# Kernel optimization log

Measured on AMD Instinct MI355X. Metric: run time of the kernel, lower is better.

## Reference

```python
import jax, jax.numpy as jnp
import numpy as np

GH, GW, H, B, IN = 4, 2, 512, 8192, 1
FC_HID = H // 2
NC = GH * GW
BN_EPS = 1e-5


def setup_inputs() -> dict:
    key = jax.random.key(0)
    ks = jax.random.split(key, 20)
    def n(k, shape, s=1.0):
        return jax.random.normal(k, shape, dtype=jnp.float32) * s
    return {
        "x": n(ks[0], (B, GH, GW)),
        "h_ext": n(ks[1], (B, H), 0.1),
        "c_ext": n(ks[2], (B, H), 0.1),
        "grid_h": n(ks[3], (GH, GW, B, H), 0.1),
        "grid_c": n(ks[4], (GH, GW, B, H), 0.1),
        "Wh": n(ks[5], (NC, H, 3 * H), (3 * H) ** -0.5),
        "bh": n(ks[6], (NC, H), 0.01),
        "Wc": n(ks[7], (NC, H, 3 * H), (3 * H) ** -0.5),
        "bc": n(ks[8], (NC, H), 0.01),
        "W_ih": n(ks[9], (NC, 4 * H, IN), 1.0),
        "W_hh": n(ks[10], (NC, 4 * H, H), H ** -0.5),
        "b_ih": n(ks[11], (NC, 4 * H), 0.01),
        "b_hh": n(ks[12], (NC, 4 * H), 0.01),
        "W1": n(ks[13], (FC_HID, 2 * H), (2 * H) ** -0.5),
        "b1": n(ks[14], (FC_HID,), 0.01),
        "W2": n(ks[15], (1, FC_HID), FC_HID ** -0.5),
        "b2": n(ks[16], (1,), 0.01),
        "gamma": jnp.ones((1,), jnp.float32),
        "beta": jnp.zeros((1,), jnp.float32),
    }


def _lattice_forward(x, h_ext, c_ext, grid_h, grid_c, Wh, bh, Wc, bc,
                     W_ih, W_hh, b_ih, b_hh, W1, b1, W2, b2, gamma, beta):
    b = x.shape[0]
    zeros = jnp.zeros((b, H), x.dtype)
    # python lists over the small fixed 4x2 grid (strict left/up dependency)
    sh = [[grid_h[i, j] for j in range(GW)] for i in range(GH)]
    sc = [[grid_c[i, j] for j in range(GW)] for i in range(GH)]
    for i in range(GH):
        for j in range(GW):
            k = i * GW + j
            h_prev, c_prev = sh[i][j], sc[i][j]
            if i == 0 and j == 0:
                h_left, c_left = h_ext, c_ext
            elif j > 0:
                h_left, c_left = sh[i][j - 1], sc[i][j - 1]
            else:
                h_left, c_left = zeros, zeros
            if i > 0:
                h_up, c_up = sh[i - 1][j], sc[i - 1][j]
            else:
                h_up, c_up = zeros, zeros
            comb_h = jnp.concatenate([h_left, h_up, h_prev], axis=1)  # [B,3H]
            comb_c = jnp.concatenate([c_left, c_up, c_prev], axis=1)
            ph = comb_h @ Wh[k].T + bh[k]  # [B,H]
            pc = comb_c @ Wc[k].T + bc[k]
            xi = x[:, i, j][:, None]  # [B,1]
            gates = xi @ W_ih[k].T + b_ih[k] + ph @ W_hh[k].T + b_hh[k]  # [B,4H]
            ig, fg, gg, og = jnp.split(gates, 4, axis=1)
            c_new = jax.nn.sigmoid(fg) * pc + jax.nn.sigmoid(ig) * jnp.tanh(gg)
            h_new = jax.nn.sigmoid(og) * jnp.tanh(c_new)
            sh[i][j], sc[i][j] = h_new, c_new
    final_h = sh[-1][-1] + h_ext
    final_c = sc[-1][-1] + c_ext
    final = jnp.concatenate([final_h, final_c], axis=1)  # [B,2H]
    hid = jax.nn.relu(final @ W1.T + b1)
    out = hid @ W2.T + b2  # [B,1]
    # BatchNorm1d in training mode: biased batch stats over the batch dim
    mu = jnp.mean(out, axis=0, keepdims=True)
    var = jnp.mean((out - mu) ** 2, axis=0, keepdims=True)
    out = gamma * (out - mu) * jax.lax.rsqrt(var + BN_EPS) + beta
    out = jax.nn.sigmoid(out)
    new_gh = jnp.stack([jnp.stack(row) for row in sh])  # [GH,GW,B,H]
    new_gc = jnp.stack([jnp.stack(row) for row in sc])
    return out, final_h, final_c, new_gh, new_gc


def reference(x, h_ext, c_ext, grid_h, grid_c, Wh, bh, Wc, bc,
              W_ih, W_hh, b_ih, b_hh, W1, b1, W2, b2, gamma, beta):
    return _lattice_forward(x, h_ext, c_ext, grid_h, grid_c, Wh, bh, Wc, bc,
                            W_ih, W_hh, b_ih, b_hh, W1, b1, W2, b2, gamma, beta)
```

## Files before the change

### kernel.cpp

```cpp
#include <hip/hip_runtime.h>
#include <stdint.h>

#define B_SZ 8192
static const size_t BH = (size_t)B_SZ * 512;

typedef short bfrag8 __attribute__((ext_vector_type(8)));
typedef float f32x4 __attribute__((ext_vector_type(4)));

__device__ __forceinline__ unsigned short f2bf(float f) {
  union { float f; uint32_t u; } c; c.f = f;
  uint32_t u = c.u;
  uint32_t r = (u + 0x7FFFu + ((u >> 16) & 1u)) >> 16;
  return (unsigned short)r;
}
__device__ __forceinline__ float bf2f(unsigned short u) {
  union { uint32_t u; float f; } c; c.u = ((uint32_t)u) << 16;
  return c.f;
}
__device__ __forceinline__ uint32_t pk2(float a, float b) {
  uint32_t r;
  asm("v_cvt_pk_bf16_f32 %0, %1, %2" : "=v"(r) : "v"(a), "v"(b));
  return r;
}
__device__ __forceinline__ float sigm(float x) { return 1.0f / (1.0f + __expf(-x)); }
__device__ __forceinline__ float tanh_fast(float x) {
  float cx = fminf(fmaxf(x, -15.0f), 15.0f);
  float e = __expf(2.0f * cx);
  return (e - 1.0f) / (e + 1.0f);
}

__device__ __forceinline__ void gload16(const void* g, void* l) {
  __builtin_amdgcn_global_load_lds(
      (const __attribute__((address_space(1))) void*)g,
      (__attribute__((address_space(3))) void*)l, 16, 0, 0);
}

__device__ __forceinline__ void xcd_swizzle(int& bx, int& by, int& bz) {
  int nx = gridDim.x, ny = gridDim.y, nz = gridDim.z;
  int nwg = nx * ny * nz;
  int id = blockIdx.x + nx * (blockIdx.y + ny * blockIdx.z);
  int q = nwg >> 3, r = nwg & 7;
  int xcd = id & 7, lin = id >> 3;
  int swz = (xcd < r ? xcd * (q + 1) : r * (q + 1) + (xcd - r) * q) + lin;
  bx = swz % nx; swz /= nx;
  by = swz % ny; bz = swz / ny;
}

struct PJob {
  const void* A[3];
  int co[3];
  int nseg, relu;
  const unsigned short* B;
  const float* bias;
  unsigned short* outBf;
  unsigned short* outBf2;
};
struct PArgs {
  PJob j[8];
  int ldA, ldB, outStride;
};

template <int AF32>
__global__ __launch_bounds__(256, 4) void pgemm_k(PArgs pa) {
  __shared__ __align__(16) char As[16384];
  __shared__ __align__(16) char Bs[16384];
  int bx, by, bz;
  xcd_swizzle(bx, by, bz);
  const PJob jb = pa.j[bz];
  const int tid = threadIdx.x;
  const int lane = tid & 63;
  const int wv = tid >> 6;
  const int wr = wv >> 1, wc = wv & 1;
  const int m0 = by * 128;
  const int ldA = pa.ldA;

  int rowA[4], cg[4];
  const char* browPtr[4];
#pragma unroll
  for (int q = 0; q < 4; ++q) {
    int cl = q * 256 + tid;
    int row = cl >> 3, cs = cl & 7;
    cg[q] = cs ^ (row & 7);
    rowA[q] = row;
    browPtr[q] = (const char*)jb.B + (size_t)(bx * 128 + row) * pa.ldB * 2;
  }

  f32x4 acc[4][4];
#pragma unroll
  for (int a = 0; a < 4; ++a)
#pragma unroll
    for (int b = 0; b < 4; ++b) acc[a][b] = f32x4{0.f, 0.f, 0.f, 0.f};

  for (int s = 0; s < jb.nseg; ++s) {
    const int coB = jb.co[s] * 2;
    for (int k0 = 0; k0 < 512; k0 += 64) {
#pragma unroll
      for (int q = 0; q < 4; ++q)
        gload16(browPtr[q] + coB + k0 * 2 + cg[q] * 16,
                Bs + (q * 256 + tid) * 16);
      if (AF32) {
        const float* Ab = (const float*)jb.A[s];
#pragma unroll
        for (int q = 0; q < 4; ++q) {
          const float4* p = (const float4*)(Ab + (size_t)(m0 + rowA[q]) * ldA +
                                            k0 + cg[q] * 8);
          float4 a0 = p[0];
          float4 a1 = p[1];
          uint4 w;
          w.x = pk2(a0.x, a0.y);
          w.y = pk2(a0.z, a0.w);
          w.z = pk2(a1.x, a1.y);
          w.w = pk2(a1.z, a1.w);
          *(uint4*)(As + (q * 256 + tid) * 16) = w;
        }
      } else {
        const char* Ab = (const char*)jb.A[s];
#pragma unroll
        for (int q = 0; q < 4; ++q)
          gload16(Ab + ((size_t)(m0 + rowA[q]) * ldA + k0) * 2 + cg[q] * 16,
                  As + (q * 256 + tid) * 16);
      }
      __syncthreads();
#pragma unroll
      for (int ks = 0; ks < 2; ++ks) {
        bfrag8 af[4], bfr[4];
#pragma unroll
        for (int mf = 0; mf < 4; ++mf) {
          int row = wr * 64 + mf * 16 + (lane & 15);
          af[mf] = *(const bfrag8*)(As + row * 128 +
                                    ((ks * 4 + (lane >> 4)) ^ (row & 7)) * 16);
        }
#pragma unroll
        for (int nf = 0; nf < 4; ++nf) {
          int row = wc * 64 + nf * 16 + (lane & 15);
          bfr[nf] = *(const bfrag8*)(Bs + row * 128 +
                                     ((ks * 4 + (lane >> 4)) ^ (row & 7)) * 16);
        }
#pragma unroll
        for (int mf = 0; mf < 4; ++mf)
#pragma unroll
          for (int nf = 0; nf < 4; ++nf)
            acc[mf][nf] = __builtin_amdgcn_mfma_f32_16x16x32_bf16(
                af[mf], bfr[nf], acc[mf][nf], 0, 0, 0);
      }
      __syncthreads();
    }
  }

  const int c4 = lane & 15;
  const int r4 = lane >> 4;
  const int n0 = bx * 128;
#pragma unroll
  for (int nf = 0; nf < 4; ++nf) {
    int colg = n0 + wc * 64 + nf * 16 + c4;
    float bv = jb.bias[colg];
#pragma unroll
    for (int mf = 0; mf < 4; ++mf)
#pragma unroll
      for (int r = 0; r < 4; ++r) {
        int rowg = m0 + wr * 64 + mf * 16 + r4 * 4 + r;
        size_t o = (size_t)rowg * pa.outStride + colg;
        float v = acc[mf][nf][r] + bv;
        if (jb.relu) v = fmaxf(v, 0.0f);
        jb.outBf[o] = f2bf(v);
      }
  }
}

struct GJob {
  const unsigned short* ph;
  const unsigned short* Whh;
  const unsigned short* pc;
  float* gh; float* gc;
  int cell, last;
};
struct GArgs {
  GJob j[2];
  const float* x;
  const float* W_ih; const float* b_ih; const float* b_hh;
  const float* h_ext; const float* c_ext;
  float* fh; float* fc;
  unsigned short* finalB;
};

__global__ __launch_bounds__(256, 2) void gates_k(GArgs ga) {
  __shared__ __align__(16) char lds[65536];
  int bx, by, bz;
  xcd_swizzle(bx, by, bz);
  const GJob jb = ga.j[bz];
  const int tid = threadIdx.x;
  const int lane = tid & 63;
  const int wv = tid >> 6;
  const int wr = wv >> 1, wc = wv & 1;
  const int m0 = by * 128;

  int rowA[4], cg[4];
  const char* browPtr[4];
#pragma unroll
  for (int q = 0; q < 4; ++q) {
    int cl = q * 256 + tid;
    int row = cl >> 3, cs = cl & 7;
    cg[q] = cs ^ (row & 7);
    rowA[q] = row;
    int gate = (row >> 4) & 3;
    int hh = bx * 32 + ((row >> 6) << 4) + (row & 15);
    browPtr[q] = (const char*)jb.Whh + (size_t)(gate * 512 + hh) * 512 * 2;
  }

  f32x4 acc[4][4];
#pragma unroll
  for (int a = 0; a < 4; ++a)
#pragma unroll
    for (int b = 0; b < 4; ++b) acc[a][b] = f32x4{0.f, 0.f, 0.f, 0.f};

  auto stagef = [&](int t, int buf) {
    int k0 = t << 6;
    char* base = lds + buf * 32768;
#pragma unroll
    for (int q = 0; q < 4; ++q)
      gload16((const char*)jb.ph + ((size_t)(m0 + rowA[q]) * 512 + k0) * 2 + cg[q] * 16,
              base + (q * 256 + tid) * 16);
#pragma unroll
    for (int q = 0; q < 4; ++q)
      gload16(browPtr[q] + k0 * 2 + cg[q] * 16,
              base + 16384 + (q * 256 + tid) * 16);
  };

  stagef(0, 0);
  int cur = 0;
  for (int t = 0; t < 8; ++t) {
    if (t + 1 < 8) {
      stagef(t + 1, cur ^ 1);
      asm volatile("s_waitcnt vmcnt(8)" ::: "memory");
    } else {
      asm volatile("s_waitcnt vmcnt(0)" ::: "memory");
    }
    __builtin_amdgcn_s_barrier();
    asm volatile("" ::: "memory");
    const char* As = lds + cur * 32768;
    const char* Bs = As + 16384;
    __builtin_amdgcn_s_setprio(1);
#pragma unroll
    for (int ks = 0; ks < 2; ++ks) {
      bfrag8 af[4], bfr[4];
#pragma unroll
      for (int mf = 0; mf < 4; ++mf) {
        int row = wr * 64 + mf * 16 + (lane & 15);
        af[mf] = *(const bfrag8*)(As + row * 128 +
                                  ((ks * 4 + (lane >> 4)) ^ (row & 7)) * 16);
      }
#pragma unroll
      for (int nf = 0; nf < 4; ++nf) {
        int row = wc * 64 + nf * 16 + (lane & 15);
        bfr[nf] = *(const bfrag8*)(Bs + row * 128 +
                                   ((ks * 4 + (lane >> 4)) ^ (row & 7)) * 16);
      }
#pragma unroll
      for (int mf = 0; mf < 4; ++mf)
#pragma unroll
        for (int nf = 0; nf < 4; ++nf)
          acc[mf][nf] = __builtin_amdgcn_mfma_f32_16x16x32_bf16(
              af[mf], bfr[nf], acc[mf][nf], 0, 0, 0);
    }
    __builtin_amdgcn_s_setprio(0);
    asm volatile("" ::: "memory");
    __builtin_amdgcn_s_barrier();
    asm volatile("" ::: "memory");
    cur ^= 1;
  }

  const int c4 = lane & 15;
  const int r4 = lane >> 4;
  int hcol = bx * 32 + wc * 16 + c4;
  const float* Wih = ga.W_ih + jb.cell * 2048;
  const float* bih = ga.b_ih + jb.cell * 2048;
  const float* bhh = ga.b_hh + jb.cell * 2048;
  float wih[4], gb[4];
#pragma unroll
  for (int q = 0; q < 4; ++q) {
    wih[q] = Wih[q * 512 + hcol];
    gb[q] = bih[q * 512 + hcol] + bhh[q * 512 + hcol];
  }
#pragma unroll
  for (int mf = 0; mf < 4; ++mf)
#pragma unroll
    for (int r = 0; r < 4; ++r) {
      int b = m0 + wr * 64 + mf * 16 + r4 * 4 + r;
      float xi = ga.x[b * 8 + jb.cell];
      float vi = acc[mf][0][r] + xi * wih[0] + gb[0];
      float vf = acc[mf][1][r] + xi * wih[1] + gb[1];
      float vg = acc[mf][2][r] + xi * wih[2] + gb[2];
      float vo = acc[mf][3][r] + xi * wih[3] + gb[3];
      size_t o = (size_t)b * 512 + hcol;
      float pcv = bf2f(jb.pc[o]);
      float cn = sigm(vf) * pcv + sigm(vi) * tanh_fast(vg);
      float hn = sigm(vo) * tanh_fast(cn);
      jb.gh[o] = hn;
      jb.gc[o] = cn;
      if (jb.last) {
        float fh = hn + ga.h_ext[o];
        float fc = cn + ga.c_ext[o];
        ga.fh[o] = fh;
        ga.fc[o] = fc;
        ga.finalB[(size_t)b * 1024 + hcol] = f2bf(fh);
        ga.finalB[(size_t)b * 1024 + 512 + hcol] = f2bf(fc);
      }
    }
}

struct CvtArgs {
  const float4* s[8];
  uint2* d[8];
  long start[9];
};
__global__ __launch_bounds__(256) void convert_many(CvtArgs ca) {
  long total = ca.start[8];
  long stride = (long)gridDim.x * blockDim.x;
  for (long idx = (long)blockIdx.x * blockDim.x + threadIdx.x; idx < total;
       idx += stride) {
    int jb = 0;
#pragma unroll
    for (int q = 1; q < 8; ++q) jb += (idx >= ca.start[q]) ? 1 : 0;
    long local = idx - ca.start[jb];
    float4 v = ca.s[jb][local];
    uint2 o;
    o.x = (uint32_t)f2bf(v.x) | ((uint32_t)f2bf(v.y) << 16);
    o.y = (uint32_t)f2bf(v.z) | ((uint32_t)f2bf(v.w) << 16);
    ca.d[jb][local] = o;
  }
}

__global__ __launch_bounds__(256)
void fc2_kernel(const unsigned short* hid, const float* W2, const float* b2,
                float* outlin) {
  int row = blockIdx.x * 4 + (threadIdx.x >> 6);
  int lane = threadIdx.x & 63;
  uint2 hv = ((const uint2*)(hid + (size_t)row * 256))[lane];
  float4 wv = ((const float4*)W2)[lane];
  float s = bf2f((unsigned short)(hv.x & 0xffffu)) * wv.x +
            bf2f((unsigned short)(hv.x >> 16)) * wv.y +
            bf2f((unsigned short)(hv.y & 0xffffu)) * wv.z +
            bf2f((unsigned short)(hv.y >> 16)) * wv.w;
#pragma unroll
  for (int o = 32; o > 0; o >>= 1) s += __shfl_down(s, o);
  if (lane == 0) outlin[row] = s + b2[0];
}

__global__ __launch_bounds__(1024)
void bn_kernel(const float* outlin, const float* gamma, const float* beta,
               float* out) {
  __shared__ float sred[16], sred2[16];
  __shared__ float smu, srs;
  float s = 0.f, s2 = 0.f;
  for (int i = threadIdx.x; i < 8192; i += 1024) {
    float v = outlin[i];
    s += v; s2 += v * v;
  }
#pragma unroll
  for (int o = 32; o > 0; o >>= 1) { s += __shfl_down(s, o); s2 += __shfl_down(s2, o); }
  if ((threadIdx.x & 63) == 0) { sred[threadIdx.x >> 6] = s; sred2[threadIdx.x >> 6] = s2; }
  __syncthreads();
  if (threadIdx.x == 0) {
    float S = 0.f, S2 = 0.f;
    for (int q = 0; q < 16; ++q) { S += sred[q]; S2 += sred2[q]; }
    float mu = S * (1.0f / 8192.0f);
    float var = S2 * (1.0f / 8192.0f) - mu * mu;
    smu = mu; srs = rsqrtf(var + 1e-5f);
  }
  __syncthreads();
  float gm = gamma[0], bt = beta[0];
  for (int i = threadIdx.x; i < 8192; i += 1024) {
    float v = (outlin[i] - smu) * srs * gm + bt;
    out[i] = sigm(v);
  }
}

extern "C" void kernel_launch(void* const* d_in, const int* in_sizes, int n_in,
                              void* d_out, int out_size, void* d_ws, size_t ws_size,
                              hipStream_t stream) {
  const float* x      = (const float*)d_in[0];
  const float* h_ext  = (const float*)d_in[1];
  const float* c_ext  = (const float*)d_in[2];
  const float* grid_h = (const float*)d_in[3];
  const float* grid_c = (const float*)d_in[4];
  const float* Wh     = (const float*)d_in[5];
  const float* bh     = (const float*)d_in[6];
  const float* Wc     = (const float*)d_in[7];
  const float* bc     = (const float*)d_in[8];
  const float* W_ih   = (const float*)d_in[9];
  const float* W_hh   = (const float*)d_in[10];
  const float* b_ih   = (const float*)d_in[11];
  const float* b_hh   = (const float*)d_in[12];
  const float* W1     = (const float*)d_in[13];
  const float* b1     = (const float*)d_in[14];
  const float* W2     = (const float*)d_in[15];
  const float* b2     = (const float*)d_in[16];
  const float* gamma  = (const float*)d_in[17];
  const float* beta   = (const float*)d_in[18];

  float* out = (float*)d_out;
  float* fh_out = out + 8192;
  float* fc_out = fh_out + BH;
  float* gh_out = fc_out + BH;
  float* gc_out = gh_out + 8 * BH;

  char* ws = (char*)d_ws;
  size_t off = 0;
  auto alloc = [&](size_t bytes) {
    char* p = ws + off;
    off = (off + bytes + 255) & ~(size_t)255;
    return p;
  };
  unsigned short* whB   = (unsigned short*)alloc(8ull * 512 * 1536 * 2);
  unsigned short* wcB   = (unsigned short*)alloc(8ull * 512 * 1536 * 2);
  unsigned short* whhB  = (unsigned short*)alloc(8ull * 2048 * 512 * 2);
  unsigned short* w1B   = (unsigned short*)alloc(256ull * 1024 * 2);
  unsigned short* pcB   = (unsigned short*)alloc(8 * BH * 2);
  unsigned short* phB   = (unsigned short*)alloc(8 * BH * 2);
  unsigned short* finalB = (unsigned short*)alloc((size_t)B_SZ * 1024 * 2);
  unsigned short* hidB   = (unsigned short*)alloc((size_t)B_SZ * 256 * 2);
  float*          outlin = (float*)alloc((size_t)B_SZ * 4);

  {
    CvtArgs ca;
    long n4[4] = {8L * 512 * 1536 / 4, 8L * 512 * 1536 / 4,
                  8L * 2048 * 512 / 4, 256L * 1024 / 4};
    const float* srcs[4] = {Wh, Wc, W_hh, W1};
    unsigned short* dsts[4] = {whB, wcB, whhB, w1B};
    ca.start[0] = 0;
    for (int q = 0; q < 8; ++q) {
      int qq = q < 4 ? q : 3;
      ca.s[q] = (const float4*)srcs[qq];
      ca.d[q] = (uint2*)dsts[qq];
      ca.start[q + 1] = ca.start[q] + (q < 4 ? n4[q] : 0);
    }
    convert_many<<<2048, 256, 0, stream>>>(ca);
  }

  auto launch_p = [&](const int* cells, int n) {
    PArgs pa = {};
    pa.ldA = 512; pa.ldB = 1536; pa.outStride = 512;
    for (int q = 0; q < n; ++q) {
      int k = cells[q];
      int i = k >> 1, jj = k & 1;
      PJob& jh = pa.j[2 * q];
      PJob& jc = pa.j[2 * q + 1];
      jh = PJob{}; jc = PJob{};
      int ns = 0;
      if (k == 0) {
        jh.A[ns] = h_ext; jc.A[ns] = c_ext;
        jh.co[ns] = 0; jc.co[ns] = 0; ns++;
      } else if (jj > 0) {
        jh.A[ns] = gh_out + (size_t)(k - 1) * BH;
        jc.A[ns] = gc_out + (size_t)(k - 1) * BH;
        jh.co[ns] = 0; jc.co[ns] = 0; ns++;
      }
      if (i > 0) {
        jh.A[ns] = gh_out + (size_t)(k - 2) * BH;
        jc.A[ns] = gc_out + (size_t)(k - 2) * BH;
        jh.co[ns] = 512; jc.co[ns] = 512; ns++;
      }
      jh.A[ns] = grid_h + (size_t)k * BH;
      jc.A[ns] = grid_c + (size_t)k * BH;
      jh.co[ns] = 1024; jc.co[ns] = 1024; ns++;
      jh.nseg = ns; jc.nseg = ns;
      jh.B = whB + (size_t)k * 512 * 1536; jh.bias = bh + k * 512;
      jc.B = wcB + (size_t)k * 512 * 1536; jc.bias = bc + k * 512;
      jh.outBf = phB + (size_t)k * BH;
      jc.outBf = pcB + (size_t)k * BH;
    }
    pgemm_k<1><<<dim3(4, 64, 2 * n), 256, 0, stream>>>(pa);
  };

  auto launch_gates = [&](const int* cells, int n) {
    GArgs ga = {};
    ga.x = x; ga.W_ih = W_ih; ga.b_ih = b_ih; ga.b_hh = b_hh;
    ga.h_ext = h_ext; ga.c_ext = c_ext;
    ga.fh = fh_out; ga.fc = fc_out; ga.finalB = finalB;
    for (int q = 0; q < n; ++q) {
      int k = cells[q];
      GJob& j = ga.j[q];
      j.ph = phB + (size_t)k * BH;
      j.Whh = whhB + (size_t)k * 2048 * 512;
      j.pc = pcB + (size_t)k * BH;
      j.gh = gh_out + (size_t)k * BH;
      j.gc = gc_out + (size_t)k * BH;
      j.cell = k; j.last = (k == 7);
    }
    gates_k<<<dim3(16, 64, n), 256, 0, stream>>>(ga);
  };

  const int diags[5][2] = {{0, -1}, {1, 2}, {3, 4}, {5, 6}, {7, -1}};
  const int dn[5] = {1, 2, 2, 2, 1};
  for (int d = 0; d < 5; ++d) {
    launch_p(diags[d], dn[d]);
    launch_gates(diags[d], dn[d]);
  }

  {
    PArgs pa = {};
    pa.ldA = 1024; pa.ldB = 1024; pa.outStride = 256;
    PJob& j = pa.j[0];
    j = PJob{};
    j.A[0] = finalB; j.co[0] = 0;
    j.A[1] = finalB + 512; j.co[1] = 512;
    j.nseg = 2; j.relu = 1;
    j.B = w1B; j.bias = b1; j.outBf = hidB;
    pgemm_k<0><<<dim3(2, 64, 1), 256, 0, stream>>>(pa);
  }

  fc2_kernel<<<2048, 256, 0, stream>>>(hidB, W2, b2, outlin);
  bn_kernel<<<1, 1024, 0, stream>>>(outlin, gamma, beta, out);
}
```

Before: 752.4 us.

## Enlarge gates GEMM tile to 256x256 with 512 threads and dynamic LDS

The gates kernel now uses 8 waves per block, each computing a 128x64 subtile, so one block covers 256 batch rows by 64 hidden columns (all four gates). This raises operand reuse and cuts the number of global loads per FLOP. It uses 128KB of dynamic LDS for double buffering and 128 accumulator registers per thread, which limits occupancy. The wait/barrier schedule changes to a full vmcnt(0) wait after compute, and setprio is dropped. The unused outBf2 field is also removed.

```diff
diff --git a/kernel.cpp b/kernel.cpp
--- a/kernel.cpp
+++ b/kernel.cpp
@@ -53,7 +53,6 @@
   const unsigned short* B;
   const float* bias;
   unsigned short* outBf;
-  unsigned short* outBf2;
 };
 struct PArgs {
   PJob j[8];
@@ -183,87 +182,85 @@
   unsigned short* finalB;
 };
 
-__global__ __launch_bounds__(256, 2) void gates_k(GArgs ga) {
-  __shared__ __align__(16) char lds[65536];
+__global__ __launch_bounds__(512, 2) void gates_k(GArgs ga) {
+  extern __shared__ char lds[];
   int bx, by, bz;
   xcd_swizzle(bx, by, bz);
   const GJob jb = ga.j[bz];
   const int tid = threadIdx.x;
   const int lane = tid & 63;
   const int wv = tid >> 6;
-  const int wr = wv >> 1, wc = wv & 1;
-  const int m0 = by * 128;
-
-  int rowA[4], cg[4];
-  const char* browPtr[4];
+  const int wr = wv >> 2;
+  const int wc = wv & 3;
+  const int m0 = by * 256;
+
+  int rowS[4], cgS[4];
+  const char* bPtr[4];
 #pragma unroll
   for (int q = 0; q < 4; ++q) {
-    int cl = q * 256 + tid;
+    int cl = q * 512 + tid;
     int row = cl >> 3, cs = cl & 7;
-    cg[q] = cs ^ (row & 7);
-    rowA[q] = row;
-    int gate = (row >> 4) & 3;
-    int hh = bx * 32 + ((row >> 6) << 4) + (row & 15);
-    browPtr[q] = (const char*)jb.Whh + (size_t)(gate * 512 + hh) * 512 * 2;
-  }
-
-  f32x4 acc[4][4];
-#pragma unroll
-  for (int a = 0; a < 4; ++a)
+    cgS[q] = cs ^ (row & 7);
+    rowS[q] = row;
+    int browG = ((row >> 4) & 3) * 512 + bx * 64 + ((row >> 6) << 4) + (row & 15);
+    bPtr[q] = (const char*)jb.Whh + (size_t)browG * 512 * 2;
+  }
+
+  auto stage = [&](int t, int buf) {
+    int k0 = t << 6;
+    char* Ab = lds + buf * 32768;
+    char* Bb = lds + 65536 + buf * 32768;
+#pragma unroll
+    for (int q = 0; q < 4; ++q)
+      gload16((const char*)jb.ph + ((size_t)(m0 + rowS[q]) * 512 + k0) * 2 + cgS[q] * 16,
+              Ab + (q * 512 + tid) * 16);
+#pragma unroll
+    for (int q = 0; q < 4; ++q)
+      gload16(bPtr[q] + k0 * 2 + cgS[q] * 16, Bb + (q * 512 + tid) * 16);
+  };
+
+  f32x4 acc[8][4];
+#pragma unroll
+  for (int a = 0; a < 8; ++a)
 #pragma unroll
     for (int b = 0; b < 4; ++b) acc[a][b] = f32x4{0.f, 0.f, 0.f, 0.f};
 
-  auto stagef = [&](int t, int buf) {
-    int k0 = t << 6;
-    char* base = lds + buf * 32768;
-#pragma unroll
-    for (int q = 0; q < 4; ++q)
-      gload16((const char*)jb.ph + ((size_t)(m0 + rowA[q]) * 512 + k0) * 2 + cg[q] * 16,
-              base + (q * 256 + tid) * 16);
-#pragma unroll
-    for (int q = 0; q < 4; ++q)
-      gload16(browPtr[q] + k0 * 2 + cg[q] * 16,
-              base + 16384 + (q * 256 + tid) * 16);
-  };
-
-  stagef(0, 0);
+  stage(0, 0);
+  asm volatile("s_waitcnt vmcnt(0)" ::: "memory");
+  __builtin_amdgcn_s_barrier();
+  asm volatile("" ::: "memory");
+
   int cur = 0;
   for (int t = 0; t < 8; ++t) {
-    if (t + 1 < 8) {
-      stagef(t + 1, cur ^ 1);
-      asm volatile("s_waitcnt vmcnt(8)" ::: "memory");
-    } else {
-      asm volatile("s_waitcnt vmcnt(0)" ::: "memory");
+    if (t + 1 < 8) stage(t + 1, cur ^ 1);
+    const char* As = lds + cur * 32768;
+    const char* Bs = lds + 65536 + cur * 32768;
+    bfrag8 bfr[4][2];
+#pragma unroll
+    for (int nf = 0; nf < 4; ++nf)
+#pragma unroll
+      for (int ks = 0; ks < 2; ++ks) {
+        int row = wc * 64 + nf * 16 + (lane & 15);
+        bfr[nf][ks] = *(const bfrag8*)(Bs + row * 128 +
+                                       (((ks * 4 + (lane >> 4)) ^ (row & 7)) * 16));
+      }
+#pragma unroll
+    for (int mf = 0; mf < 8; ++mf) {
+      bfrag8 af[2];
+#pragma unroll
+      for (int ks = 0; ks < 2; ++ks) {
+        int row = wr * 128 + mf * 16 + (lane & 15);
+        af[ks] = *(const bfrag8*)(As + row * 128 +
+                                  (((ks * 4 + (lane >> 4)) ^ (row & 7)) * 16));
+      }
+#pragma unroll
+      for (int nf = 0; nf < 4; ++nf)
+#pragma unroll
+        for (int ks = 0; ks < 2; ++ks)
+          acc[mf][nf] = __builtin_amdgcn_mfma_f32_16x16x32_bf16(
+              af[ks], bfr[nf][ks], acc[mf][nf], 0, 0, 0);
     }
-    __builtin_amdgcn_s_barrier();
-    asm volatile("" ::: "memory");
-    const char* As = lds + cur * 32768;
-    const char* Bs = As + 16384;
-    __builtin_amdgcn_s_setprio(1);
-#pragma unroll
-    for (int ks = 0; ks < 2; ++ks) {
-      bfrag8 af[4], bfr[4];
-#pragma unroll
-      for (int mf = 0; mf < 4; ++mf) {
-        int row = wr * 64 + mf * 16 + (lane & 15);
-        af[mf] = *(const bfrag8*)(As + row * 128 +
-                                  ((ks * 4 + (lane >> 4)) ^ (row & 7)) * 16);
-      }
-#pragma unroll
-      for (int nf = 0; nf < 4; ++nf) {
-        int row = wc * 64 + nf * 16 + (lane & 15);
-        bfr[nf] = *(const bfrag8*)(Bs + row * 128 +
-                                   ((ks * 4 + (lane >> 4)) ^ (row & 7)) * 16);
-      }
-#pragma unroll
-      for (int mf = 0; mf < 4; ++mf)
-#pragma unroll
-        for (int nf = 0; nf < 4; ++nf)
-          acc[mf][nf] = __builtin_amdgcn_mfma_f32_16x16x32_bf16(
-              af[mf], bfr[nf], acc[mf][nf], 0, 0, 0);
-    }
-    __builtin_amdgcn_s_setprio(0);
-    asm volatile("" ::: "memory");
+    asm volatile("s_waitcnt vmcnt(0)" ::: "memory");
     __builtin_amdgcn_s_barrier();
     asm volatile("" ::: "memory");
     cur ^= 1;
@@ -271,7 +268,7 @@
 
   const int c4 = lane & 15;
   const int r4 = lane >> 4;
-  int hcol = bx * 32 + wc * 16 + c4;
+  int hcol = bx * 64 + wc * 16 + c4;
   const float* Wih = ga.W_ih + jb.cell * 2048;
   const float* bih = ga.b_ih + jb.cell * 2048;
   const float* bhh = ga.b_hh + jb.cell * 2048;
@@ -282,10 +279,10 @@
     gb[q] = bih[q * 512 + hcol] + bhh[q * 512 + hcol];
   }
 #pragma unroll
-  for (int mf = 0; mf < 4; ++mf)
+  for (int mf = 0; mf < 8; ++mf)
 #pragma unroll
     for (int r = 0; r < 4; ++r) {
-      int b = m0 + wr * 64 + mf * 16 + r4 * 4 + r;
+      int b = m0 + wr * 128 + mf * 16 + r4 * 4 + r;
       float xi = ga.x[b * 8 + jb.cell];
       float vi = acc[mf][0][r] + xi * wih[0] + gb[0];
       float vf = acc[mf][1][r] + xi * wih[1] + gb[1];
@@ -421,6 +418,9 @@
   unsigned short* hidB   = (unsigned short*)alloc((size_t)B_SZ * 256 * 2);
   float*          outlin = (float*)alloc((size_t)B_SZ * 4);
 
+  hipFuncSetAttribute((const void*)gates_k,
+                      hipFuncAttributeMaxDynamicSharedMemorySize, 131072);
+
   {
     CvtArgs ca;
     long n4[4] = {8L * 512 * 1536 / 4, 8L * 512 * 1536 / 4,
@@ -487,7 +487,7 @@
       j.gc = gc_out + (size_t)k * BH;
       j.cell = k; j.last = (k == 7);
     }
-    gates_k<<<dim3(16, 64, n), 256, 0, stream>>>(ga);
+    gates_k<<<dim3(8, 32, n), 512, 131072, stream>>>(ga);
   };
 
   const int diags[5][2] = {{0, -1}, {1, 2}, {3, 4}, {5, 6}, {7, -1}};
```

Measured after the change: 732.9 us. 1.03x faster.
